# Optimization experiments

Hardware: AMD Instinct MI355X
Metric: run time of the kernel (lower is better)

The kernel has to match this reference:

```python
import jax, jax.numpy as jnp
import numpy as np

N_NODES = 100000
N_EDGES = 1600000


def setup_inputs() -> dict:
    key = jax.random.key(0)
    k1, k2, k3, k4, k5 = jax.random.split(key, 5)
    node_states = jax.random.normal(k1, (N_NODES, 128), dtype=jnp.float32)
    edge_index = jax.random.randint(k2, (2, N_EDGES), 0, N_NODES, dtype=jnp.int64)
    mask = jax.random.uniform(k3, (N_EDGES,), dtype=jnp.float32)  # edge weights
    # Glorot-ish init for the two GCN linear layers
    W1 = jax.random.normal(k4, (128, 64), dtype=jnp.float32) * 0.05
    b1 = jnp.zeros((64,), dtype=jnp.float32)
    W2 = jax.random.normal(k5, (64, 64), dtype=jnp.float32) * 0.05
    b2 = jnp.zeros((64,), dtype=jnp.float32)
    return {"node_states": node_states, "edge_index": edge_index, "mask": mask,
            "W1": W1, "b1": b1, "W2": W2, "b2": b2}


def _gcn_layer(x, src, dst, edge_w, W, b, n_nodes):
    # PyG GCNConv (normalize=False): h = x @ W; out[dst] += edge_w * h[src]; out += b
    h = x @ W                                  # [N, d_out]
    msg = h[src] * edge_w[:, None]             # [E, d_out] gather + scale
    agg = jax.ops.segment_sum(msg, dst, num_segments=n_nodes)  # scatter-add
    return agg + b


def reference(node_states, edge_index, mask, W1, b1, W2, b2):
    src = edge_index[0]
    dst = edge_index[1]
    n = node_states.shape[0]
    h1 = jax.nn.relu(_gcn_layer(node_states, src, dst, mask, W1, b1, n))
    h2 = jax.nn.relu(_gcn_layer(h1, src, dst, mask, W2, b2, n))
    return h2
```

## Files before the change

### kernel.cpp

```cpp
#include <hip/hip_runtime.h>
#include <hip/hip_bf16.h>

#define N_NODES 100000
#define N_EDGES 1600000
#define NBUCKET 391
#define NBLK 640
#define CHUNK_E 2500
#define T2 (NBUCKET * NBLK)
#define NCH2 ((T2 + 511) / 512)

typedef short v8s __attribute__((ext_vector_type(8)));
typedef float v4f __attribute__((ext_vector_type(4)));

static __device__ __forceinline__ unsigned pack_bf2(float a, float b) {
    __hip_bfloat162 p = __float22bfloat162_rn(make_float2(a, b));
    return *reinterpret_cast<unsigned*>(&p);
}
static __device__ __forceinline__ float2 bf2_to_f2(unsigned u) {
    __hip_bfloat162 p = *reinterpret_cast<__hip_bfloat162*>(&u);
    return __bfloat1622float2(p);
}

__global__ __launch_bounds__(256) void prep_w(const float* __restrict__ W1,
                                              const float* __restrict__ W2,
                                              short* __restrict__ wt1,
                                              short* __restrict__ wt2) {
    const int t = threadIdx.x;
    for (int i = t; i < 64 * 128; i += 256) {
        const int c = i >> 7, k = i & 127;
        wt1[i] = (short)(pack_bf2(W1[k * 64 + c], 0.f) & 0xFFFF);
    }
    for (int i = t; i < 64 * 64; i += 256) {
        const int c = i >> 6, k = i & 63;
        wt2[i] = (short)(pack_bf2(W2[k * 64 + c], 0.f) & 0xFFFF);
    }
}

template<int K, bool IN_BF>
__global__ __launch_bounds__(256) void gemm_mfma(const void* __restrict__ in,
                                                 const short* __restrict__ wt,
                                                 unsigned* __restrict__ outp) {
    __shared__ unsigned xs[64][K / 2 + 4];
    __shared__ unsigned ws[64][K / 2 + 4];
    const int t = threadIdx.x;
    const int row0 = blockIdx.x * 64;
    {
        const uint2* g = (const uint2*)wt;
        for (int i = t; i < 64 * K / 4; i += 256) {
            const int r = i / (K / 4), cu = i % (K / 4);
            ((uint2*)&ws[r][0])[cu] = g[i];
        }
    }
    if (IN_BF) {
        const uint2* g = (const uint2*)in;
        for (int i = t; i < 64 * K / 4; i += 256) {
            const int r = i / (K / 4), cu = i % (K / 4);
            const int row = row0 + r;
            uint2 v = make_uint2(0u, 0u);
            if (row < N_NODES) v = g[(size_t)row * (K / 4) + cu];
            ((uint2*)&xs[r][0])[cu] = v;
        }
    } else {
        const float4* g = (const float4*)in;
        for (int i = t; i < 64 * K / 4; i += 256) {
            const int r = i / (K / 4), cu = i % (K / 4);
            const int row = row0 + r;
            uint2 v = make_uint2(0u, 0u);
            if (row < N_NODES) {
                float4 f = g[(size_t)row * (K / 4) + cu];
                v.x = pack_bf2(f.x, f.y);
                v.y = pack_bf2(f.z, f.w);
            }
            ((uint2*)&xs[r][0])[cu] = v;
        }
    }
    __syncthreads();
    const int w = t >> 6;
    const int lane = t & 63;
    const int l15 = lane & 15;
    const int quad = lane >> 4;
    v4f acc[4];
#pragma unroll
    for (int tt = 0; tt < 4; ++tt) acc[tt] = (v4f){0.f, 0.f, 0.f, 0.f};
#pragma unroll
    for (int k0 = 0; k0 < K; k0 += 32) {
        const int ku = k0 / 2 + quad * 4;
        const v8s xb = *(const v8s*)&xs[w * 16 + l15][ku];
#pragma unroll
        for (int tt = 0; tt < 4; ++tt) {
            const v8s wa = *(const v8s*)&ws[16 * tt + l15][ku];
            acc[tt] = __builtin_amdgcn_mfma_f32_16x16x32_bf16(wa, xb, acc[tt], 0, 0, 0);
        }
    }
    const int node = row0 + w * 16 + l15;
    if (node < N_NODES) {
#pragma unroll
        for (int tt = 0; tt < 4; ++tt) {
            uint2 o;
            o.x = pack_bf2(acc[tt][0], acc[tt][1]);
            o.y = pack_bf2(acc[tt][2], acc[tt][3]);
            *(uint2*)&outp[(size_t)node * 32 + 8 * tt + 2 * quad] = o;
        }
    }
}

__global__ __launch_bounds__(256) void s1_hist(const int* __restrict__ dst,
                                               int* __restrict__ bh) {
    __shared__ int hist[NBUCKET];
    const int t = threadIdx.x;
    for (int i = t; i < NBUCKET; i += 256) hist[i] = 0;
    __syncthreads();
    const int4* d4 = (const int4*)(dst + blockIdx.x * CHUNK_E);
    for (int i = t; i < CHUNK_E / 4; i += 256) {
        const int4 v = d4[i];
        atomicAdd(&hist[v.x >> 8], 1);
        atomicAdd(&hist[v.y >> 8], 1);
        atomicAdd(&hist[v.z >> 8], 1);
        atomicAdd(&hist[v.w >> 8], 1);
    }
    __syncthreads();
    for (int i = t; i < NBUCKET; i += 256)
        bh[i * NBLK + blockIdx.x] = hist[i];
}

__global__ __launch_bounds__(256) void scan_sums(const int* __restrict__ v,
                                                 int* __restrict__ csum, int n) {
    __shared__ int red[256];
    const int t = threadIdx.x;
    const int i0 = blockIdx.x * 512 + 2 * t;
    int a = (i0 < n) ? v[i0] : 0;
    int b = (i0 + 1 < n) ? v[i0 + 1] : 0;
    red[t] = a + b;
    __syncthreads();
    for (int off = 128; off > 0; off >>= 1) {
        if (t < off) red[t] += red[t + off];
        __syncthreads();
    }
    if (t == 0) csum[blockIdx.x] = red[0];
}

__global__ __launch_bounds__(512) void scan_off(const int* __restrict__ csum,
                                                int* __restrict__ coff, int nch) {
    __shared__ int part[512];
    const int t = threadIdx.x;
    int v = (t < nch) ? csum[t] : 0;
    part[t] = v;
    __syncthreads();
    for (int off = 1; off < 512; off <<= 1) {
        int u = (t >= off) ? part[t - off] : 0;
        __syncthreads();
        part[t] += u;
        __syncthreads();
    }
    if (t < nch) coff[t] = part[t] - v;
}

__global__ __launch_bounds__(256) void scan_apply(const int* __restrict__ v,
                                                  const int* __restrict__ coff,
                                                  int* __restrict__ vex, int n) {
    __shared__ int part[256];
    const int t = threadIdx.x;
    const int i0 = blockIdx.x * 512 + 2 * t;
    int a = (i0 < n) ? v[i0] : 0;
    int b = (i0 + 1 < n) ? v[i0 + 1] : 0;
    int pair = a + b;
    part[t] = pair;
    __syncthreads();
    for (int off = 1; off < 256; off <<= 1) {
        int u = (t >= off) ? part[t - off] : 0;
        __syncthreads();
        part[t] += u;
        __syncthreads();
    }
    const int e0 = coff[blockIdx.x] + part[t] - pair;
    if (i0 < n)     vex[i0] = e0;
    if (i0 + 1 < n) vex[i0 + 1] = e0 + a;
}

__global__ __launch_bounds__(256) void s3_scatter(const int* __restrict__ src,
                                                  const int* __restrict__ dst,
                                                  const float* __restrict__ w,
                                                  const int* __restrict__ bh_ex,
                                                  int2* __restrict__ coarse) {
    __shared__ int cur[NBUCKET];
    const int t = threadIdx.x;
    for (int i = t; i < NBUCKET; i += 256) cur[i] = bh_ex[i * NBLK + blockIdx.x];
    __syncthreads();
    const int e0 = blockIdx.x * CHUNK_E;
    const int4*   s4 = (const int4*)(src + e0);
    const int4*   d4 = (const int4*)(dst + e0);
    const float4* w4 = (const float4*)(w + e0);
    for (int i = t; i < CHUNK_E / 4; i += 256) {
        const int4 sv = s4[i];
        const int4 dv = d4[i];
        const float4 wv = w4[i];
        {
            const int pos = atomicAdd(&cur[dv.x >> 8], 1);
            coarse[pos] = make_int2(sv.x | ((dv.x & 255) << 17), __float_as_int(wv.x));
        }
        {
            const int pos = atomicAdd(&cur[dv.y >> 8], 1);
            coarse[pos] = make_int2(sv.y | ((dv.y & 255) << 17), __float_as_int(wv.y));
        }
        {
            const int pos = atomicAdd(&cur[dv.z >> 8], 1);
            coarse[pos] = make_int2(sv.z | ((dv.z & 255) << 17), __float_as_int(wv.z));
        }
        {
            const int pos = atomicAdd(&cur[dv.w >> 8], 1);
            coarse[pos] = make_int2(sv.w | ((dv.w & 255) << 17), __float_as_int(wv.w));
        }
    }
}

__global__ __launch_bounds__(256) void s4_fine(const int2* __restrict__ coarse,
                                               const int* __restrict__ bh_ex,
                                               unsigned* __restrict__ edge_sorted,
                                               int* __restrict__ row_ptr) {
    __shared__ int hist[256];
    __shared__ int part[256];
    __shared__ int cursor[256];
    const int b = blockIdx.x;
    const int t = threadIdx.x;
    const int beg = bh_ex[b * NBLK];
    const int end = (b + 1 < NBUCKET) ? bh_ex[(b + 1) * NBLK] : N_EDGES;
    hist[t] = 0;
    __syncthreads();
    for (int i = beg + t; i < end; i += 256)
        atomicAdd(&hist[(coarse[i].x >> 17) & 255], 1);
    __syncthreads();
    const int v = hist[t];
    part[t] = v;
    __syncthreads();
    for (int off = 1; off < 256; off <<= 1) {
        int u = (t >= off) ? part[t - off] : 0;
        __syncthreads();
        part[t] += u;
        __syncthreads();
    }
    const int excl = beg + part[t] - v;
    cursor[t] = excl;
    const int node = b * 256 + t;
    if (node < N_NODES) row_ptr[node] = excl;
    if (b == NBUCKET - 1 && t == 0) row_ptr[N_NODES] = N_EDGES;
    __syncthreads();
    for (int i = beg + t; i < end; i += 256) {
        const int2 ev = coarse[i];
        const int f = (ev.x >> 17) & 255;
        const int pos = atomicAdd(&cursor[f], 1);
        unsigned wq = (unsigned)__float2uint_rn(__int_as_float(ev.y) * 32767.f);
        wq = min(wq, 32767u);
        edge_sorted[pos] = (unsigned)(ev.x & 0x1FFFF) | (wq << 17);
    }
}

template<bool FULL>
static __device__ __forceinline__ void octo_step(const unsigned* __restrict__ h,
                                                 const unsigned* __restrict__ recs,
                                                 int e, int n, int q, int cg,
                                                 float acc[8]) {
    unsigned u;
    if (FULL) {
        u = recs[e + q];
    } else {
        u = recs[e + min(q, n - 1)];
    }
    const int sx = u & 0x1FFFF;
    float wq = (float)(u >> 17) * (1.f / 32767.f);
    if (!FULL) wq = (q < n) ? wq : 0.f;
    const uint4 hv = *(const uint4*)&h[(size_t)sx * 32 + cg * 4];
    const float2 f0 = bf2_to_f2(hv.x);
    const float2 f1 = bf2_to_f2(hv.y);
    const float2 f2 = bf2_to_f2(hv.z);
    const float2 f3 = bf2_to_f2(hv.w);
    acc[0] += wq * f0.x; acc[1] += wq * f0.y;
    acc[2] += wq * f1.x; acc[3] += wq * f1.y;
    acc[4] += wq * f2.x; acc[5] += wq * f2.y;
    acc[6] += wq * f3.x; acc[7] += wq * f3.y;
}

template<bool OUT_BF>
__global__ __launch_bounds__(256) void gather_octo(const unsigned* __restrict__ h,
                                                   const int* __restrict__ row_ptr,
                                                   const unsigned* __restrict__ recs,
                                                   const float* __restrict__ bias,
                                                   void* __restrict__ outp) {
    const int node = (blockIdx.x * 256 + threadIdx.x) >> 6;
    if (node >= N_NODES) return;
    const int lane = threadIdx.x & 63;
    const int q  = lane >> 3;
    const int cg = lane & 7;
    const int beg = __builtin_amdgcn_readfirstlane(row_ptr[node]);
    const int end = __builtin_amdgcn_readfirstlane(row_ptr[node + 1]);
    float acc[8];
#pragma unroll
    for (int i = 0; i < 8; ++i) acc[i] = 0.f;
    int e = beg;
    for (; e + 16 <= end; e += 16) {
        octo_step<true>(h, recs, e, 8, q, cg, acc);
        octo_step<true>(h, recs, e + 8, 8, q, cg, acc);
    }
    if (e + 8 <= end) {
        octo_step<true>(h, recs, e, 8, q, cg, acc);
        e += 8;
    }
    if (e < end) {
        octo_step<false>(h, recs, e, end - e, q, cg, acc);
    }
    const bool h8 = (lane & 8) != 0;
    const float t0 = __shfl_xor(h8 ? acc[0] : acc[4], 8);
    const float t1 = __shfl_xor(h8 ? acc[1] : acc[5], 8);
    const float t2 = __shfl_xor(h8 ? acc[2] : acc[6], 8);
    const float t3 = __shfl_xor(h8 ? acc[3] : acc[7], 8);
    const float a0 = (h8 ? acc[4] : acc[0]) + t0;
    const float a1 = (h8 ? acc[5] : acc[1]) + t1;
    const float a2 = (h8 ? acc[6] : acc[2]) + t2;
    const float a3 = (h8 ? acc[7] : acc[3]) + t3;
    const bool h16 = (lane & 16) != 0;
    const float u0 = __shfl_xor(h16 ? a0 : a2, 16);
    const float u1 = __shfl_xor(h16 ? a1 : a3, 16);
    const float b0 = (h16 ? a2 : a0) + u0;
    const float b1 = (h16 ? a3 : a1) + u1;
    const bool h32 = (lane & 32) != 0;
    const float v0 = __shfl_xor(h32 ? b0 : b1, 32);
    const float rsum = (h32 ? b1 : b0) + v0;
    const int colq = ((q & 1) << 2) | (q & 2) | ((q >> 2) & 1);
    const int col = 8 * cg + colq;
    const float r = fmaxf(rsum + bias[col], 0.f);
    if (OUT_BF) {
        const unsigned p = pack_bf2(r, 0.f);
        ((short*)outp)[(size_t)node * 64 + col] = (short)(p & 0xFFFF);
    } else {
        ((float*)outp)[(size_t)node * 64 + col] = r;
    }
}

extern "C" void kernel_launch(void* const* d_in, const int* in_sizes, int n_in,
                              void* d_out, int out_size, void* d_ws, size_t ws_size,
                              hipStream_t stream) {
    const float* x    = (const float*)d_in[0];
    const int*   eidx = (const int*)d_in[1];
    const float* mask = (const float*)d_in[2];
    const float* W1   = (const float*)d_in[3];
    const float* b1   = (const float*)d_in[4];
    const float* W2   = (const float*)d_in[5];
    const float* b2   = (const float*)d_in[6];
    float* out = (float*)d_out;

    const int* src = eidx;
    const int* dst = eidx + N_EDGES;

    unsigned* hpre     = (unsigned*)d_ws;
    unsigned* edge_sorted = (unsigned*)(hpre + (size_t)N_NODES * 32);
    int2*  coarse      = (int2*)(edge_sorted + N_EDGES);
    unsigned* h1bf     = (unsigned*)coarse;
    int*   bh          = (int*)(coarse + N_EDGES);
    int*   bh_ex       = bh + T2;
    int*   csum2       = bh_ex + T2;
    int*   coff2       = csum2 + NCH2;
    int*   row_ptr     = coff2 + NCH2;
    short* wt1         = (short*)(row_ptr + N_NODES + 1);
    short* wt2         = wt1 + 64 * 128;

    const int gemmBlocks = (N_NODES + 63) / 64;
    const int gatherBlocks = (N_NODES * 64 + 255) / 256;

    prep_w<<<1, 256, 0, stream>>>(W1, W2, wt1, wt2);

    s1_hist<<<NBLK, 256, 0, stream>>>(dst, bh);
    scan_sums<<<NCH2, 256, 0, stream>>>(bh, csum2, T2);
    scan_off<<<1, 512, 0, stream>>>(csum2, coff2, NCH2);
    scan_apply<<<NCH2, 256, 0, stream>>>(bh, coff2, bh_ex, T2);
    s3_scatter<<<NBLK, 256, 0, stream>>>(src, dst, mask, bh_ex, coarse);
    s4_fine<<<NBUCKET, 256, 0, stream>>>(coarse, bh_ex, edge_sorted, row_ptr);

    gemm_mfma<128, false><<<gemmBlocks, 256, 0, stream>>>(x, wt1, hpre);
    gather_octo<true><<<gatherBlocks, 256, 0, stream>>>(hpre, row_ptr, edge_sorted,
                                                        b1, h1bf);

    gemm_mfma<64, true><<<gemmBlocks, 256, 0, stream>>>(h1bf, wt2, hpre);
    gather_octo<false><<<gatherBlocks, 256, 0, stream>>>(hpre, row_ptr, edge_sorted,
                                                         b2, out);
}
```

Before: 255.0 us.

## Slice feature columns into four passes to shrink gather working set

The GEMM output is stored column-sliced, four slices of 16 bf16 features laid out contiguously per node. Each gather then runs as four separate passes, one per slice, so the random-access gather table per pass (100k nodes × 32B, about 3.2MB) is more likely to stay resident in cache. Edge records use nontemporal loads and outputs use nontemporal stores. The weight-prep kernel is folded into the histogram launch as an extra block. In exchange, the edge list is read four times per layer and there are more kernel launches.

```diff
diff --git a/kernel.cpp b/kernel.cpp
--- a/kernel.cpp
+++ b/kernel.cpp
@@ -21,22 +21,41 @@
     return __bfloat1622float2(p);
 }
 
-__global__ __launch_bounds__(256) void prep_w(const float* __restrict__ W1,
-                                              const float* __restrict__ W2,
-                                              short* __restrict__ wt1,
-                                              short* __restrict__ wt2) {
-    const int t = threadIdx.x;
-    for (int i = t; i < 64 * 128; i += 256) {
-        const int c = i >> 7, k = i & 127;
-        wt1[i] = (short)(pack_bf2(W1[k * 64 + c], 0.f) & 0xFFFF);
-    }
-    for (int i = t; i < 64 * 64; i += 256) {
-        const int c = i >> 6, k = i & 63;
-        wt2[i] = (short)(pack_bf2(W2[k * 64 + c], 0.f) & 0xFFFF);
-    }
-}
-
-template<int K, bool IN_BF>
+__global__ __launch_bounds__(256) void s1_hist_prep(const int* __restrict__ dst,
+                                                    int* __restrict__ bh,
+                                                    const float* __restrict__ W1,
+                                                    const float* __restrict__ W2,
+                                                    short* __restrict__ wt1,
+                                                    short* __restrict__ wt2) {
+    const int t = threadIdx.x;
+    if (blockIdx.x == NBLK) {
+        for (int i = t; i < 64 * 128; i += 256) {
+            const int c = i >> 7, k = i & 127;
+            wt1[i] = (short)(pack_bf2(W1[k * 64 + c], 0.f) & 0xFFFF);
+        }
+        for (int i = t; i < 64 * 64; i += 256) {
+            const int c = i >> 6, k = i & 63;
+            wt2[i] = (short)(pack_bf2(W2[k * 64 + c], 0.f) & 0xFFFF);
+        }
+        return;
+    }
+    __shared__ int hist[NBUCKET];
+    for (int i = t; i < NBUCKET; i += 256) hist[i] = 0;
+    __syncthreads();
+    const int4* d4 = (const int4*)(dst + blockIdx.x * CHUNK_E);
+    for (int i = t; i < CHUNK_E / 4; i += 256) {
+        const int4 v = d4[i];
+        atomicAdd(&hist[v.x >> 8], 1);
+        atomicAdd(&hist[v.y >> 8], 1);
+        atomicAdd(&hist[v.z >> 8], 1);
+        atomicAdd(&hist[v.w >> 8], 1);
+    }
+    __syncthreads();
+    for (int i = t; i < NBUCKET; i += 256)
+        bh[i * NBLK + blockIdx.x] = hist[i];
+}
+
+template<int K, bool IN_SLICED>
 __global__ __launch_bounds__(256) void gemm_mfma(const void* __restrict__ in,
                                                  const short* __restrict__ wt,
                                                  unsigned* __restrict__ outp) {
@@ -51,13 +70,13 @@
             ((uint2*)&ws[r][0])[cu] = g[i];
         }
     }
-    if (IN_BF) {
+    if (IN_SLICED) {
         const uint2* g = (const uint2*)in;
         for (int i = t; i < 64 * K / 4; i += 256) {
             const int r = i / (K / 4), cu = i % (K / 4);
             const int row = row0 + r;
             uint2 v = make_uint2(0u, 0u);
-            if (row < N_NODES) v = g[(size_t)row * (K / 4) + cu];
+            if (row < N_NODES) v = g[((size_t)(cu >> 2) * N_NODES + row) * 4 + (cu & 3)];
             ((uint2*)&xs[r][0])[cu] = v;
         }
     } else {
@@ -99,28 +118,9 @@
             uint2 o;
             o.x = pack_bf2(acc[tt][0], acc[tt][1]);
             o.y = pack_bf2(acc[tt][2], acc[tt][3]);
-            *(uint2*)&outp[(size_t)node * 32 + 8 * tt + 2 * quad] = o;
-        }
-    }
-}
-
-__global__ __launch_bounds__(256) void s1_hist(const int* __restrict__ dst,
-                                               int* __restrict__ bh) {
-    __shared__ int hist[NBUCKET];
-    const int t = threadIdx.x;
-    for (int i = t; i < NBUCKET; i += 256) hist[i] = 0;
-    __syncthreads();
-    const int4* d4 = (const int4*)(dst + blockIdx.x * CHUNK_E);
-    for (int i = t; i < CHUNK_E / 4; i += 256) {
-        const int4 v = d4[i];
-        atomicAdd(&hist[v.x >> 8], 1);
-        atomicAdd(&hist[v.y >> 8], 1);
-        atomicAdd(&hist[v.z >> 8], 1);
-        atomicAdd(&hist[v.w >> 8], 1);
-    }
-    __syncthreads();
-    for (int i = t; i < NBUCKET; i += 256)
-        bh[i * NBLK + blockIdx.x] = hist[i];
+            *(uint2*)&outp[((size_t)tt * N_NODES + node) * 8 + 2 * quad] = o;
+        }
+    }
 }
 
 __global__ __launch_bounds__(256) void scan_sums(const int* __restrict__ v,
@@ -255,83 +255,76 @@
 }
 
 template<bool FULL>
-static __device__ __forceinline__ void octo_step(const unsigned* __restrict__ h,
+static __device__ __forceinline__ void quad_step(const unsigned* __restrict__ hs,
                                                  const unsigned* __restrict__ recs,
-                                                 int e, int n, int q, int cg,
-                                                 float acc[8]) {
+                                                 int e, int n, int eq, int cg,
+                                                 float acc[4]) {
     unsigned u;
     if (FULL) {
-        u = recs[e + q];
+        u = __builtin_nontemporal_load(&recs[e + eq]);
     } else {
-        u = recs[e + min(q, n - 1)];
+        u = __builtin_nontemporal_load(&recs[e + min(eq, n - 1)]);
     }
     const int sx = u & 0x1FFFF;
     float wq = (float)(u >> 17) * (1.f / 32767.f);
-    if (!FULL) wq = (q < n) ? wq : 0.f;
-    const uint4 hv = *(const uint4*)&h[(size_t)sx * 32 + cg * 4];
+    if (!FULL) wq = (eq < n) ? wq : 0.f;
+    const uint2 hv = *(const uint2*)&hs[(size_t)sx * 8 + cg * 2];
     const float2 f0 = bf2_to_f2(hv.x);
     const float2 f1 = bf2_to_f2(hv.y);
-    const float2 f2 = bf2_to_f2(hv.z);
-    const float2 f3 = bf2_to_f2(hv.w);
     acc[0] += wq * f0.x; acc[1] += wq * f0.y;
     acc[2] += wq * f1.x; acc[3] += wq * f1.y;
-    acc[4] += wq * f2.x; acc[5] += wq * f2.y;
-    acc[6] += wq * f3.x; acc[7] += wq * f3.y;
 }
 
 template<bool OUT_BF>
-__global__ __launch_bounds__(256) void gather_octo(const unsigned* __restrict__ h,
+__global__ __launch_bounds__(256) void gather_pass(const unsigned* __restrict__ hs,
                                                    const int* __restrict__ row_ptr,
                                                    const unsigned* __restrict__ recs,
                                                    const float* __restrict__ bias,
-                                                   void* __restrict__ outp) {
+                                                   void* __restrict__ outp,
+                                                   int p) {
     const int node = (blockIdx.x * 256 + threadIdx.x) >> 6;
     if (node >= N_NODES) return;
     const int lane = threadIdx.x & 63;
-    const int q  = lane >> 3;
-    const int cg = lane & 7;
+    const int eq = lane >> 2;
+    const int cg = lane & 3;
     const int beg = __builtin_amdgcn_readfirstlane(row_ptr[node]);
     const int end = __builtin_amdgcn_readfirstlane(row_ptr[node + 1]);
-    float acc[8];
-#pragma unroll
-    for (int i = 0; i < 8; ++i) acc[i] = 0.f;
+    float acc[4];
+#pragma unroll
+    for (int i = 0; i < 4; ++i) acc[i] = 0.f;
     int e = beg;
-    for (; e + 16 <= end; e += 16) {
-        octo_step<true>(h, recs, e, 8, q, cg, acc);
-        octo_step<true>(h, recs, e + 8, 8, q, cg, acc);
-    }
-    if (e + 8 <= end) {
-        octo_step<true>(h, recs, e, 8, q, cg, acc);
-        e += 8;
+    for (; e + 32 <= end; e += 32) {
+        quad_step<true>(hs, recs, e, 16, eq, cg, acc);
+        quad_step<true>(hs, recs, e + 16, 16, eq, cg, acc);
+    }
+    if (e + 16 <= end) {
+        quad_step<true>(hs, recs, e, 16, eq, cg, acc);
+        e += 16;
     }
     if (e < end) {
-        octo_step<false>(h, recs, e, end - e, q, cg, acc);
-    }
+        quad_step<false>(hs, recs, e, end - e, eq, cg, acc);
+    }
+    const bool h4 = (lane & 4) != 0;
+    const float t0 = __shfl_xor(h4 ? acc[0] : acc[2], 4);
+    const float t1 = __shfl_xor(h4 ? acc[1] : acc[3], 4);
+    const float a0 = (h4 ? acc[2] : acc[0]) + t0;
+    const float a1 = (h4 ? acc[3] : acc[1]) + t1;
     const bool h8 = (lane & 8) != 0;
-    const float t0 = __shfl_xor(h8 ? acc[0] : acc[4], 8);
-    const float t1 = __shfl_xor(h8 ? acc[1] : acc[5], 8);
-    const float t2 = __shfl_xor(h8 ? acc[2] : acc[6], 8);
-    const float t3 = __shfl_xor(h8 ? acc[3] : acc[7], 8);
-    const float a0 = (h8 ? acc[4] : acc[0]) + t0;
-    const float a1 = (h8 ? acc[5] : acc[1]) + t1;
-    const float a2 = (h8 ? acc[6] : acc[2]) + t2;
-    const float a3 = (h8 ? acc[7] : acc[3]) + t3;
-    const bool h16 = (lane & 16) != 0;
-    const float u0 = __shfl_xor(h16 ? a0 : a2, 16);
-    const float u1 = __shfl_xor(h16 ? a1 : a3, 16);
-    const float b0 = (h16 ? a2 : a0) + u0;
-    const float b1 = (h16 ? a3 : a1) + u1;
-    const bool h32 = (lane & 32) != 0;
-    const float v0 = __shfl_xor(h32 ? b0 : b1, 32);
-    const float rsum = (h32 ? b1 : b0) + v0;
-    const int colq = ((q & 1) << 2) | (q & 2) | ((q >> 2) & 1);
-    const int col = 8 * cg + colq;
-    const float r = fmaxf(rsum + bias[col], 0.f);
-    if (OUT_BF) {
-        const unsigned p = pack_bf2(r, 0.f);
-        ((short*)outp)[(size_t)node * 64 + col] = (short)(p & 0xFFFF);
-    } else {
-        ((float*)outp)[(size_t)node * 64 + col] = r;
+    const float u0 = __shfl_xor(h8 ? a0 : a1, 8);
+    float b0 = (h8 ? a1 : a0) + u0;
+    b0 += __shfl_xor(b0, 16);
+    b0 += __shfl_xor(b0, 32);
+    if (lane < 16) {
+        const int col = 4 * cg + (h4 ? 2 : 0) + (h8 ? 1 : 0);
+        const float r = fmaxf(b0 + bias[p * 16 + col], 0.f);
+        if (OUT_BF) {
+            const unsigned pk = pack_bf2(r, 0.f);
+            __builtin_nontemporal_store((short)(pk & 0xFFFF),
+                &((short*)outp)[((size_t)p * N_NODES + node) * 16 + col]);
+        } else {
+            __builtin_nontemporal_store(r,
+                &((float*)outp)[(size_t)node * 64 + p * 16 + col]);
+        }
     }
 }
 
@@ -365,9 +358,7 @@
     const int gemmBlocks = (N_NODES + 63) / 64;
     const int gatherBlocks = (N_NODES * 64 + 255) / 256;
 
-    prep_w<<<1, 256, 0, stream>>>(W1, W2, wt1, wt2);
-
-    s1_hist<<<NBLK, 256, 0, stream>>>(dst, bh);
+    s1_hist_prep<<<NBLK + 1, 256, 0, stream>>>(dst, bh, W1, W2, wt1, wt2);
     scan_sums<<<NCH2, 256, 0, stream>>>(bh, csum2, T2);
     scan_off<<<1, 512, 0, stream>>>(csum2, coff2, NCH2);
     scan_apply<<<NCH2, 256, 0, stream>>>(bh, coff2, bh_ex, T2);
@@ -375,10 +366,12 @@
     s4_fine<<<NBUCKET, 256, 0, stream>>>(coarse, bh_ex, edge_sorted, row_ptr);
 
     gemm_mfma<128, false><<<gemmBlocks, 256, 0, stream>>>(x, wt1, hpre);
-    gather_octo<true><<<gatherBlocks, 256, 0, stream>>>(hpre, row_ptr, edge_sorted,
-                                                        b1, h1bf);
+    for (int p = 0; p < 4; ++p)
+        gather_pass<true><<<gatherBlocks, 256, 0, stream>>>(hpre + (size_t)p * N_NODES * 8,
+                                                            row_ptr, edge_sorted, b1, h1bf, p);
 
     gemm_mfma<64, true><<<gemmBlocks, 256, 0, stream>>>(h1bf, wt2, hpre);
-    gather_octo<false><<<gatherBlocks, 256, 0, stream>>>(hpre, row_ptr, edge_sorted,
-                                                         b2, out);
-}
+    for (int p = 0; p < 4; ++p)
+        gather_pass<false><<<gatherBlocks, 256, 0, stream>>>(hpre + (size_t)p * N_NODES * 8,
+                                                             row_ptr, edge_sorted, b2, out, p);
+}
```

Result: slower. 444.0 us (+74.1%).

## Fuse sort histogram, scatter and layer-1 GEMM into one kernel with atomic bucket arenas

Applied to the files above, without the earlier changes.

Replaces the global multi-kernel scan of per-block bucket histograms with per-bucket global atomic counters into fixed-capacity arena slots. Histogram and scatter are merged into one kernel, and that same launch also runs the layer-1 GEMM tiles as extra blocks. Weight conversion moves into each GEMM tile, so the prep kernel goes away. This cuts kernel launches from about 10 to 5 and removes the scan passes. In exchange, edge order within a bucket is no longer deterministic, so float summation order can vary between runs. It also relies on every bucket staying under CAP edges, which random inputs satisfy but skewed graphs may not.

```diff
diff --git a/kernel.cpp b/kernel.cpp
--- a/kernel.cpp
+++ b/kernel.cpp
@@ -6,8 +6,8 @@
 #define NBUCKET 391
 #define NBLK 640
 #define CHUNK_E 2500
-#define T2 (NBUCKET * NBLK)
-#define NCH2 ((T2 + 511) / 512)
+#define CAP 4608
+#define GCSTRIDE 32
 
 typedef short v8s __attribute__((ext_vector_type(8)));
 typedef float v4f __attribute__((ext_vector_type(4)));
@@ -21,34 +21,23 @@
     return __bfloat1622float2(p);
 }
 
-__global__ __launch_bounds__(256) void prep_w(const float* __restrict__ W1,
-                                              const float* __restrict__ W2,
-                                              short* __restrict__ wt1,
-                                              short* __restrict__ wt2) {
+template<int K, bool IN_BF>
+static __device__ __forceinline__ void gemm_tile(const void* __restrict__ in,
+                                                 const float* __restrict__ W,
+                                                 unsigned* __restrict__ outp,
+                                                 int tile, unsigned* smem) {
+    unsigned (*xs)[K / 2 + 4] = (unsigned(*)[K / 2 + 4])smem;
+    unsigned (*ws)[K / 2 + 4] = (unsigned(*)[K / 2 + 4])(smem + 64 * (K / 2 + 4));
     const int t = threadIdx.x;
-    for (int i = t; i < 64 * 128; i += 256) {
-        const int c = i >> 7, k = i & 127;
-        wt1[i] = (short)(pack_bf2(W1[k * 64 + c], 0.f) & 0xFFFF);
-    }
-    for (int i = t; i < 64 * 64; i += 256) {
-        const int c = i >> 6, k = i & 63;
-        wt2[i] = (short)(pack_bf2(W2[k * 64 + c], 0.f) & 0xFFFF);
-    }
-}
-
-template<int K, bool IN_BF>
-__global__ __launch_bounds__(256) void gemm_mfma(const void* __restrict__ in,
-                                                 const short* __restrict__ wt,
-                                                 unsigned* __restrict__ outp) {
-    __shared__ unsigned xs[64][K / 2 + 4];
-    __shared__ unsigned ws[64][K / 2 + 4];
-    const int t = threadIdx.x;
-    const int row0 = blockIdx.x * 64;
+    const int row0 = tile * 64;
     {
-        const uint2* g = (const uint2*)wt;
-        for (int i = t; i < 64 * K / 4; i += 256) {
-            const int r = i / (K / 4), cu = i % (K / 4);
-            ((uint2*)&ws[r][0])[cu] = g[i];
+        const float2* g2 = (const float2*)W;
+        for (int i = t; i < 64 * K / 2; i += 256) {
+            const float2 v = g2[i];
+            const int k = (2 * i) >> 6;
+            const int c = (2 * i) & 63;
+            ((short*)&ws[c][0])[k]     = (short)(pack_bf2(v.x, 0.f) & 0xFFFF);
+            ((short*)&ws[c + 1][0])[k] = (short)(pack_bf2(v.y, 0.f) & 0xFFFF);
         }
     }
     if (IN_BF) {
@@ -104,13 +93,26 @@
     }
 }
 
-__global__ __launch_bounds__(256) void s1_hist(const int* __restrict__ dst,
-                                               int* __restrict__ bh) {
+__global__ __launch_bounds__(256) void k1_sort_gemm(const int* __restrict__ src,
+                                                    const int* __restrict__ dst,
+                                                    const float* __restrict__ wgt,
+                                                    const float* __restrict__ x,
+                                                    const float* __restrict__ W1,
+                                                    int* __restrict__ gcount,
+                                                    int2* __restrict__ arena,
+                                                    unsigned* __restrict__ hpre) {
+    __shared__ unsigned smem[2 * 64 * (128 / 2 + 4)];
     __shared__ int hist[NBUCKET];
+    __shared__ int cur[NBUCKET];
+    const int b = blockIdx.x;
+    if (b >= NBLK) {
+        gemm_tile<128, false>(x, W1, hpre, b - NBLK, smem);
+        return;
+    }
     const int t = threadIdx.x;
     for (int i = t; i < NBUCKET; i += 256) hist[i] = 0;
     __syncthreads();
-    const int4* d4 = (const int4*)(dst + blockIdx.x * CHUNK_E);
+    const int4* d4 = (const int4*)(dst + b * CHUNK_E);
     for (int i = t; i < CHUNK_E / 4; i += 256) {
         const int4 v = d4[i];
         atomicAdd(&hist[v.x >> 8], 1);
@@ -119,52 +121,74 @@
         atomicAdd(&hist[v.w >> 8], 1);
     }
     __syncthreads();
-    for (int i = t; i < NBUCKET; i += 256)
-        bh[i * NBLK + blockIdx.x] = hist[i];
-}
-
-__global__ __launch_bounds__(256) void scan_sums(const int* __restrict__ v,
-                                                 int* __restrict__ csum, int n) {
-    __shared__ int red[256];
+    for (int i = t; i < NBUCKET; i += 256) {
+        const int h = hist[i];
+        const int base = (h > 0) ? atomicAdd(&gcount[i * GCSTRIDE], h) : 0;
+        cur[i] = i * CAP + base;
+    }
+    __syncthreads();
+    const int4*   s4p = (const int4*)(src + b * CHUNK_E);
+    const float4* w4  = (const float4*)(wgt + b * CHUNK_E);
+    for (int i = t; i < CHUNK_E / 4; i += 256) {
+        const int4 sv = s4p[i];
+        const int4 dv = d4[i];
+        const float4 wv = w4[i];
+        {
+            const int pos = atomicAdd(&cur[dv.x >> 8], 1);
+            arena[pos] = make_int2(sv.x | ((dv.x & 255) << 17), __float_as_int(wv.x));
+        }
+        {
+            const int pos = atomicAdd(&cur[dv.y >> 8], 1);
+            arena[pos] = make_int2(sv.y | ((dv.y & 255) << 17), __float_as_int(wv.y));
+        }
+        {
+            const int pos = atomicAdd(&cur[dv.z >> 8], 1);
+            arena[pos] = make_int2(sv.z | ((dv.z & 255) << 17), __float_as_int(wv.z));
+        }
+        {
+            const int pos = atomicAdd(&cur[dv.w >> 8], 1);
+            arena[pos] = make_int2(sv.w | ((dv.w & 255) << 17), __float_as_int(wv.w));
+        }
+    }
+}
+
+__global__ __launch_bounds__(256) void gemm2_k(const unsigned* __restrict__ h1bf,
+                                               const float* __restrict__ W2,
+                                               unsigned* __restrict__ hpre) {
+    __shared__ unsigned smem[2 * 64 * (64 / 2 + 4)];
+    gemm_tile<64, true>(h1bf, W2, hpre, blockIdx.x, smem);
+}
+
+__global__ __launch_bounds__(256) void s4_fine(const int2* __restrict__ arena,
+                                               const int* __restrict__ gcount,
+                                               unsigned* __restrict__ edge_sorted,
+                                               int* __restrict__ row_ptr) {
+    __shared__ int hist[256];
+    __shared__ int part[256];
+    __shared__ int cursor[256];
+    __shared__ int sb[2];
+    const int b = blockIdx.x;
     const int t = threadIdx.x;
-    const int i0 = blockIdx.x * 512 + 2 * t;
-    int a = (i0 < n) ? v[i0] : 0;
-    int b = (i0 + 1 < n) ? v[i0 + 1] : 0;
-    red[t] = a + b;
+    int partial = 0;
+    for (int i = t; i < b; i += 256) partial += gcount[i * GCSTRIDE];
+    part[t] = partial;
     __syncthreads();
     for (int off = 128; off > 0; off >>= 1) {
-        if (t < off) red[t] += red[t + off];
+        if (t < off) part[t] += part[t + off];
         __syncthreads();
     }
-    if (t == 0) csum[blockIdx.x] = red[0];
-}
-
-__global__ __launch_bounds__(512) void scan_off(const int* __restrict__ csum,
-                                                int* __restrict__ coff, int nch) {
-    __shared__ int part[512];
-    const int t = threadIdx.x;
-    int v = (t < nch) ? csum[t] : 0;
+    if (t == 0) { sb[0] = part[0]; sb[1] = gcount[b * GCSTRIDE]; }
+    __syncthreads();
+    const int gbase = sb[0];
+    const int cnt   = sb[1];
+    const int abeg  = b * CAP;
+    hist[t] = 0;
+    __syncthreads();
+    for (int i = t; i < cnt; i += 256)
+        atomicAdd(&hist[(arena[abeg + i].x >> 17) & 255], 1);
+    __syncthreads();
+    const int v = hist[t];
     part[t] = v;
-    __syncthreads();
-    for (int off = 1; off < 512; off <<= 1) {
-        int u = (t >= off) ? part[t - off] : 0;
-        __syncthreads();
-        part[t] += u;
-        __syncthreads();
-    }
-    if (t < nch) coff[t] = part[t] - v;
-}
-
-__global__ __launch_bounds__(256) void scan_apply(const int* __restrict__ v,
-                                                  const int* __restrict__ coff,
-                                                  int* __restrict__ vex, int n) {
-    __shared__ int part[256];
-    const int t = threadIdx.x;
-    const int i0 = blockIdx.x * 512 + 2 * t;
-    int a = (i0 < n) ? v[i0] : 0;
-    int b = (i0 + 1 < n) ? v[i0 + 1] : 0;
-    int pair = a + b;
-    part[t] = pair;
     __syncthreads();
     for (int off = 1; off < 256; off <<= 1) {
         int u = (t >= off) ? part[t - off] : 0;
@@ -172,80 +196,14 @@
         part[t] += u;
         __syncthreads();
     }
-    const int e0 = coff[blockIdx.x] + part[t] - pair;
-    if (i0 < n)     vex[i0] = e0;
-    if (i0 + 1 < n) vex[i0 + 1] = e0 + a;
-}
-
-__global__ __launch_bounds__(256) void s3_scatter(const int* __restrict__ src,
-                                                  const int* __restrict__ dst,
-                                                  const float* __restrict__ w,
-                                                  const int* __restrict__ bh_ex,
-                                                  int2* __restrict__ coarse) {
-    __shared__ int cur[NBUCKET];
-    const int t = threadIdx.x;
-    for (int i = t; i < NBUCKET; i += 256) cur[i] = bh_ex[i * NBLK + blockIdx.x];
-    __syncthreads();
-    const int e0 = blockIdx.x * CHUNK_E;
-    const int4*   s4 = (const int4*)(src + e0);
-    const int4*   d4 = (const int4*)(dst + e0);
-    const float4* w4 = (const float4*)(w + e0);
-    for (int i = t; i < CHUNK_E / 4; i += 256) {
-        const int4 sv = s4[i];
-        const int4 dv = d4[i];
-        const float4 wv = w4[i];
-        {
-            const int pos = atomicAdd(&cur[dv.x >> 8], 1);
-            coarse[pos] = make_int2(sv.x | ((dv.x & 255) << 17), __float_as_int(wv.x));
-        }
-        {
-            const int pos = atomicAdd(&cur[dv.y >> 8], 1);
-            coarse[pos] = make_int2(sv.y | ((dv.y & 255) << 17), __float_as_int(wv.y));
-        }
-        {
-            const int pos = atomicAdd(&cur[dv.z >> 8], 1);
-            coarse[pos] = make_int2(sv.z | ((dv.z & 255) << 17), __float_as_int(wv.z));
-        }
-        {
-            const int pos = atomicAdd(&cur[dv.w >> 8], 1);
-            coarse[pos] = make_int2(sv.w | ((dv.w & 255) << 17), __float_as_int(wv.w));
-        }
-    }
-}
-
-__global__ __launch_bounds__(256) void s4_fine(const int2* __restrict__ coarse,
-                                               const int* __restrict__ bh_ex,
-                                               unsigned* __restrict__ edge_sorted,
-                                               int* __restrict__ row_ptr) {
-    __shared__ int hist[256];
-    __shared__ int part[256];
-    __shared__ int cursor[256];
-    const int b = blockIdx.x;
-    const int t = threadIdx.x;
-    const int beg = bh_ex[b * NBLK];
-    const int end = (b + 1 < NBUCKET) ? bh_ex[(b + 1) * NBLK] : N_EDGES;
-    hist[t] = 0;
-    __syncthreads();
-    for (int i = beg + t; i < end; i += 256)
-        atomicAdd(&hist[(coarse[i].x >> 17) & 255], 1);
-    __syncthreads();
-    const int v = hist[t];
-    part[t] = v;
-    __syncthreads();
-    for (int off = 1; off < 256; off <<= 1) {
-        int u = (t >= off) ? part[t - off] : 0;
-        __syncthreads();
-        part[t] += u;
-        __syncthreads();
-    }
-    const int excl = beg + part[t] - v;
+    const int excl = gbase + part[t] - v;
     cursor[t] = excl;
     const int node = b * 256 + t;
     if (node < N_NODES) row_ptr[node] = excl;
     if (b == NBUCKET - 1 && t == 0) row_ptr[N_NODES] = N_EDGES;
     __syncthreads();
-    for (int i = beg + t; i < end; i += 256) {
-        const int2 ev = coarse[i];
+    for (int i = t; i < cnt; i += 256) {
+        const int2 ev = arena[abeg + i];
         const int f = (ev.x >> 17) & 255;
         const int pos = atomicAdd(&cursor[f], 1);
         unsigned wq = (unsigned)__float2uint_rn(__int_as_float(ev.y) * 32767.f);
@@ -350,35 +308,25 @@
     const int* src = eidx;
     const int* dst = eidx + N_EDGES;
 
-    unsigned* hpre     = (unsigned*)d_ws;
+    unsigned* hpre        = (unsigned*)d_ws;
     unsigned* edge_sorted = (unsigned*)(hpre + (size_t)N_NODES * 32);
-    int2*  coarse      = (int2*)(edge_sorted + N_EDGES);
-    unsigned* h1bf     = (unsigned*)coarse;
-    int*   bh          = (int*)(coarse + N_EDGES);
-    int*   bh_ex       = bh + T2;
-    int*   csum2       = bh_ex + T2;
-    int*   coff2       = csum2 + NCH2;
-    int*   row_ptr     = coff2 + NCH2;
-    short* wt1         = (short*)(row_ptr + N_NODES + 1);
-    short* wt2         = wt1 + 64 * 128;
+    int2*     arena       = (int2*)(edge_sorted + N_EDGES);
+    unsigned* h1bf        = (unsigned*)arena;
+    int*      gcount      = (int*)(arena + (size_t)NBUCKET * CAP);
+    int*      row_ptr     = gcount + NBUCKET * GCSTRIDE;
 
     const int gemmBlocks = (N_NODES + 63) / 64;
     const int gatherBlocks = (N_NODES * 64 + 255) / 256;
 
-    prep_w<<<1, 256, 0, stream>>>(W1, W2, wt1, wt2);
-
-    s1_hist<<<NBLK, 256, 0, stream>>>(dst, bh);
-    scan_sums<<<NCH2, 256, 0, stream>>>(bh, csum2, T2);
-    scan_off<<<1, 512, 0, stream>>>(csum2, coff2, NCH2);
-    scan_apply<<<NCH2, 256, 0, stream>>>(bh, coff2, bh_ex, T2);
-    s3_scatter<<<NBLK, 256, 0, stream>>>(src, dst, mask, bh_ex, coarse);
-    s4_fine<<<NBUCKET, 256, 0, stream>>>(coarse, bh_ex, edge_sorted, row_ptr);
-
-    gemm_mfma<128, false><<<gemmBlocks, 256, 0, stream>>>(x, wt1, hpre);
+    hipMemsetAsync(gcount, 0, NBUCKET * GCSTRIDE * sizeof(int), stream);
+
+    k1_sort_gemm<<<NBLK + gemmBlocks, 256, 0, stream>>>(src, dst, mask, x, W1,
+                                                        gcount, arena, hpre);
+    s4_fine<<<NBUCKET, 256, 0, stream>>>(arena, gcount, edge_sorted, row_ptr);
+
     gather_octo<true><<<gatherBlocks, 256, 0, stream>>>(hpre, row_ptr, edge_sorted,
                                                         b1, h1bf);
-
-    gemm_mfma<64, true><<<gemmBlocks, 256, 0, stream>>>(h1bf, wt2, hpre);
+    gemm2_k<<<gemmBlocks, 256, 0, stream>>>(h1bf, W2, hpre);
     gather_octo<false><<<gatherBlocks, 256, 0, stream>>>(hpre, row_ptr, edge_sorted,
                                                          b2, out);
 }
```

Result: no change. 253.2 us (-0.7%).
